# Optimization experiments

Hardware: AMD Instinct MI355X
Metric: run time of the kernel (lower is better)

The kernel has to match this reference:

```python
import jax, jax.numpy as jnp
import numpy as np

N, E, C_IN, H, K = 16384, 524288, 128, 64, 64


def setup_inputs() -> dict:
    key = jax.random.key(0)
    ks = jax.random.split(key, 6)
    x = jax.random.normal(ks[0], (N, C_IN), dtype=jnp.float32)
    edge_index = jax.random.randint(ks[1], (2, E), 0, N, dtype=jnp.int32)
    edge_weight = jax.random.uniform(ks[2], (E,), dtype=jnp.float32)
    sc = lambda f: 1.0 / np.sqrt(f)
    # GCNConv lin (no bias inside lin; separate bias), Glorot-ish init
    W1 = jax.random.normal(ks[3], (C_IN, H), dtype=jnp.float32) * sc(C_IN)
    b1 = jnp.zeros((H,), jnp.float32)
    # DMoNPooling MLP: Linear(H,H) then Linear(H,K), no activation between (act=None)
    Wm1 = jax.random.normal(ks[4], (H, H), dtype=jnp.float32) * sc(H)
    bm1 = jnp.zeros((H,), jnp.float32)
    Wm2 = jax.random.normal(ks[5], (H, K), dtype=jnp.float32) * sc(H)
    bm2 = jnp.zeros((K,), jnp.float32)
    return dict(x=x, edge_index=edge_index, edge_weight=edge_weight,
                W1=W1, b1=b1, Wm1=Wm1, bm1=bm1, Wm2=Wm2, bm2=bm2)


def gcn_conv(x, edge_index, edge_weight, W, b, n):
    # GCNConv: add self-loops (weight 1), symmetric deg^-1/2 normalization,
    # aggregate messages from source (row) into target (col).
    row, col = edge_index[0], edge_index[1]
    loop = jnp.arange(n, dtype=edge_index.dtype)
    row = jnp.concatenate([row, loop])
    col = jnp.concatenate([col, loop])
    w = jnp.concatenate([edge_weight, jnp.ones((n,), edge_weight.dtype)])
    deg = jax.ops.segment_sum(w, col, num_segments=n)
    dis = jnp.where(deg > 0, jax.lax.rsqrt(deg), 0.0)
    norm = dis[row] * w * dis[col]
    xw = x @ W  # [N, H]
    out = jax.ops.segment_sum(xw[row] * norm[:, None], col, num_segments=n)
    return out + b


def dmon_pool(h, adj, Wm1, bm1, Wm2, bm2):
    # eval mode: dropout disabled
    s = jax.nn.softmax((h @ Wm1 + bm1) @ Wm2 + bm2, axis=-1)  # [N, K]
    k = s.shape[-1]
    out_adj = s.T @ (adj @ s)  # [K, K]

    # Spectral (modularity) loss; degrees = einsum('ijk->ik', adj) = column sums
    deg = adj.sum(axis=0)  # [N]
    m = deg.sum() / 2
    ca = s.T @ deg  # [K], equals degrees^T s as well (symmetric roles)
    normalizer = jnp.outer(ca, ca) / 2 / m
    spectral_loss = -jnp.trace(out_adj - normalizer) / 2 / m

    # Orthogonality loss
    ss = s.T @ s  # [K, K]
    ss_fro = jnp.sqrt(jnp.sum(ss * ss))
    i_fro = jnp.sqrt(jnp.float32(k))  # ||I_K||_F
    diff = ss / ss_fro - jnp.eye(k, dtype=ss.dtype) / i_fro
    ortho_loss = jnp.sqrt(jnp.sum(diff * diff))

    # Cluster size loss
    cluster_size = s.sum(axis=0)  # [K]
    cluster_loss = jnp.sqrt(jnp.sum(cluster_size * cluster_size)) / h.shape[0] * i_fro - 1.0

    return s, spectral_loss, ortho_loss, cluster_loss


def reference(x, edge_index, edge_weight, W1, b1, Wm1, bm1, Wm2, bm2):
    h = jax.nn.relu(gcn_conv(x, edge_index, edge_weight, W1, b1, N))
    # to_dense_adj(edge_index): dense [N, N], duplicate edges summed
    adj = jnp.zeros((N, N), h.dtype).at[edge_index[0], edge_index[1]].add(1.0)
    s, spec, ortho, clus = dmon_pool(h, adj, Wm1, bm1, Wm2, bm2)
    return s[None], spec + ortho + clus
```

## Files before the change

### kernel.cpp

```cpp
#include <hip/hip_runtime.h>
#include <hip/hip_bf16.h>

typedef float          f4  __attribute__((ext_vector_type(4)));
typedef unsigned short us4 __attribute__((ext_vector_type(4)));
typedef int            i2  __attribute__((ext_vector_type(2)));

template <typename T>
__device__ __forceinline__ T ntload(const T* p) { return __builtin_nontemporal_load(p); }

__device__ __forceinline__ unsigned short f2bf(float f) {
    unsigned u = __float_as_uint(f);
    return (unsigned short)((u + 0x7FFF + ((u >> 16) & 1)) >> 16);
}
__device__ __forceinline__ float bf2f(unsigned short h) {
    return __uint_as_float((unsigned)h << 16);
}

__global__ __launch_bounds__(256) void k_degxw(const int* __restrict__ ei,
                      const float* __restrict__ ew,
                      unsigned long long* __restrict__ deg_rep,
                      const float* __restrict__ x, const float* __restrict__ W1,
                      float* __restrict__ xw, unsigned short* __restrict__ xw16,
                      int N, int E) {
    __shared__ float w1l[128 * 64];
    __shared__ f4    xt[16][32];
    if (blockIdx.x < 2048) {
        int e = blockIdx.x * 256 + threadIdx.x;
        if (e < E) {
            int c = ntload(ei + E + e);
            float w = ntload(ew + e);
            unsigned q = (unsigned)__float2uint_rn(w * 16777216.f);
            unsigned long long p = (1ULL << 40) | (unsigned long long)q;
            atomicAdd(&deg_rep[(size_t)(blockIdx.x & 7) * N + c], p);
        }
        return;
    }
    int xbid = blockIdx.x - 2048;
    for (int t = threadIdx.x; t < 128 * 64; t += 256) w1l[t] = W1[t];
    int lane = threadIdx.x & 63;
    int wv   = threadIdx.x >> 6;
    for (int base = xbid * 16; base < N; base += 512 * 16) {
        __syncthreads();
        for (int t = threadIdx.x; t < 16 * 32; t += 256)
            ((f4*)xt)[t] = ntload((const f4*)x + (size_t)base * 32 + t);
        __syncthreads();
        int r0 = wv * 4;
        float a0 = 0.f, a1 = 0.f, a2 = 0.f, a3 = 0.f;
#pragma unroll
        for (int q = 0; q < 32; ++q) {
            f4 x0 = xt[r0][q], x1 = xt[r0 + 1][q], x2 = xt[r0 + 2][q], x3 = xt[r0 + 3][q];
            float wa = w1l[(4 * q + 0) * 64 + lane];
            float wb = w1l[(4 * q + 1) * 64 + lane];
            float wc = w1l[(4 * q + 2) * 64 + lane];
            float wd = w1l[(4 * q + 3) * 64 + lane];
            a0 = fmaf(x0.x, wa, a0); a0 = fmaf(x0.y, wb, a0); a0 = fmaf(x0.z, wc, a0); a0 = fmaf(x0.w, wd, a0);
            a1 = fmaf(x1.x, wa, a1); a1 = fmaf(x1.y, wb, a1); a1 = fmaf(x1.z, wc, a1); a1 = fmaf(x1.w, wd, a1);
            a2 = fmaf(x2.x, wa, a2); a2 = fmaf(x2.y, wb, a2); a2 = fmaf(x2.z, wc, a2); a2 = fmaf(x2.w, wd, a2);
            a3 = fmaf(x3.x, wa, a3); a3 = fmaf(x3.y, wb, a3); a3 = fmaf(x3.z, wc, a3); a3 = fmaf(x3.w, wd, a3);
        }
        int gr = base + r0;
        __builtin_nontemporal_store(a0, xw + (size_t)(gr + 0) * 64 + lane);
        __builtin_nontemporal_store(a1, xw + (size_t)(gr + 1) * 64 + lane);
        __builtin_nontemporal_store(a2, xw + (size_t)(gr + 2) * 64 + lane);
        __builtin_nontemporal_store(a3, xw + (size_t)(gr + 3) * 64 + lane);
        xw16[(size_t)(gr + 0) * 64 + lane] = f2bf(a0);
        xw16[(size_t)(gr + 1) * 64 + lane] = f2bf(a1);
        xw16[(size_t)(gr + 2) * 64 + lane] = f2bf(a2);
        xw16[(size_t)(gr + 3) * 64 + lane] = f2bf(a3);
    }
}

__global__ void k_red(const unsigned long long* __restrict__ deg_rep,
                      int* __restrict__ off_rep, int* __restrict__ cnt,
                      float* __restrict__ dis, int N) {
    int c = blockIdx.x * blockDim.x + threadIdx.x;
    if (c >= N) return;
    int run = 0;
    unsigned long long wsum = 0;
#pragma unroll
    for (int rep = 0; rep < 8; ++rep) {
        unsigned long long p = deg_rep[(size_t)rep * N + c];
        off_rep[(size_t)rep * N + c] = run;
        run += (int)(p >> 40);
        wsum += (p & ((1ULL << 40) - 1));
    }
    cnt[c] = run;
    dis[c] = rsqrtf((float)wsum * (1.f / 16777216.f) + 1.0f);
}

__global__ void k_scan(const int* __restrict__ cnt, int* __restrict__ offs, int N) {
    __shared__ int part[1024];
    int tid = threadIdx.x;
    int C = (N + 1023) / 1024;
    int base = tid * C;
    int loc[16];
    int sum = 0;
#pragma unroll
    for (int i = 0; i < 16; ++i) {
        if (i < C) {
            int idx = base + i;
            loc[i] = sum;
            sum += (idx < N) ? cnt[idx] : 0;
        }
    }
    part[tid] = sum;
    __syncthreads();
    for (int o = 1; o < 1024; o <<= 1) {
        int t = (tid >= o) ? part[tid - o] : 0;
        __syncthreads();
        part[tid] += t;
        __syncthreads();
    }
    int excl = part[tid] - sum;
#pragma unroll
    for (int i = 0; i < 16; ++i) {
        if (i < C) {
            int idx = base + i;
            if (idx < N) offs[idx] = excl + loc[i];
        }
    }
    if (tid == 1023) offs[N] = part[tid];
}

__global__ void k_bucket(const int* __restrict__ ei, const float* __restrict__ ew,
                         const float* __restrict__ dis, const int* __restrict__ offs,
                         const int* __restrict__ off_rep, int* __restrict__ cursor_rep,
                         i2* __restrict__ barr, int N, int E) {
    int e = blockIdx.x * blockDim.x + threadIdx.x;
    if (e < E) {
        int rep = blockIdx.x & 7;
        int r = ntload(ei + e), c = ntload(ei + E + e);
        float norm = dis[r] * ntload(ew + e) * dis[c];
        size_t rc = (size_t)rep * N + c;
        int pos = offs[c] + off_rep[rc] + atomicAdd(&cursor_rep[rc], 1);
        i2 rec; rec.x = r; rec.y = __float_as_int(norm);
        barr[pos] = rec;
    }
}

__global__ __launch_bounds__(512) void k_gmlp(const int* __restrict__ offs,
                         const i2* __restrict__ barr,
                         const float* __restrict__ xw, const unsigned short* __restrict__ xw16,
                         const float* __restrict__ dis, const float* __restrict__ b1,
                         const float* __restrict__ Wm1, const float* __restrict__ bm1,
                         const float* __restrict__ Wm2, const float* __restrict__ bm2,
                         float* __restrict__ s, unsigned short* __restrict__ s16, int N) {
    __shared__ float w1m[4096], w2m[4096];
    __shared__ float tsc[8][2][64];
    for (int t = threadIdx.x; t < 4096; t += 512) { w1m[t] = Wm1[t]; w2m[t] = Wm2[t]; }
    __syncthreads();
    int lane = threadIdx.x & 63;
    int sub = lane >> 4, q = lane & 15;
    int wv   = threadIdx.x >> 6;
    int wid  = blockIdx.x * 8 + wv;
    int nw   = 8 * gridDim.x;
    const us4* xw16v = (const us4*)xw16;
    for (int cp = wid; cp < (N >> 1); cp += nw) {
        int c0 = 2 * cp, c1 = c0 + 1;
        int beg = ntload(offs + c0), mid = ntload(offs + c1), end = ntload(offs + c1 + 1);
        f4 A0 = {0.f, 0.f, 0.f, 0.f}, A1 = A0, B0 = A0, B1 = A0;
        for (int i = beg; i < end; i += 64) {
            int nloc = min(64, end - i);
            bool ok = (i + lane < end);
            i2 b = ok ? ntload(barr + i + lane) : (i2){0, 0};
            int   rv = b.x;
            float nv = __int_as_float(b.y);
            int jmax = (nloc + 3) >> 2;
            int j = 0;
            for (; j + 4 <= jmax; j += 4) {
                int e0 = 4 * j + sub;
                int g0 = i + e0;
                int   r0 = __shfl(rv, e0),      r1 = __shfl(rv, e0 + 4);
                int   r2 = __shfl(rv, e0 + 8),  r3 = __shfl(rv, e0 + 12);
                float n0 = __shfl(nv, e0),      n1 = __shfl(nv, e0 + 4);
                float n2 = __shfl(nv, e0 + 8),  n3 = __shfl(nv, e0 + 12);
                us4 u0 = xw16v[(size_t)r0 * 16 + q];
                us4 u1 = xw16v[(size_t)r1 * 16 + q];
                us4 u2 = xw16v[(size_t)r2 * 16 + q];
                us4 u3 = xw16v[(size_t)r3 * 16 + q];
                float a0w = (g0      < mid) ? n0 : 0.f, b0w = n0 - a0w;
                float a1w = (g0 + 4  < mid) ? n1 : 0.f, b1w = n1 - a1w;
                float a2w = (g0 + 8  < mid) ? n2 : 0.f, b2w = n2 - a2w;
                float a3w = (g0 + 12 < mid) ? n3 : 0.f, b3w = n3 - a3w;
                A0.x = fmaf(bf2f(u0.x), a0w, A0.x); A0.y = fmaf(bf2f(u0.y), a0w, A0.y);
                A0.z = fmaf(bf2f(u0.z), a0w, A0.z); A0.w = fmaf(bf2f(u0.w), a0w, A0.w);
                B0.x = fmaf(bf2f(u0.x), b0w, B0.x); B0.y = fmaf(bf2f(u0.y), b0w, B0.y);
                B0.z = fmaf(bf2f(u0.z), b0w, B0.z); B0.w = fmaf(bf2f(u0.w), b0w, B0.w);
                A1.x = fmaf(bf2f(u1.x), a1w, A1.x); A1.y = fmaf(bf2f(u1.y), a1w, A1.y);
                A1.z = fmaf(bf2f(u1.z), a1w, A1.z); A1.w = fmaf(bf2f(u1.w), a1w, A1.w);
                B1.x = fmaf(bf2f(u1.x), b1w, B1.x); B1.y = fmaf(bf2f(u1.y), b1w, B1.y);
                B1.z = fmaf(bf2f(u1.z), b1w, B1.z); B1.w = fmaf(bf2f(u1.w), b1w, B1.w);
                A0.x = fmaf(bf2f(u2.x), a2w, A0.x); A0.y = fmaf(bf2f(u2.y), a2w, A0.y);
                A0.z = fmaf(bf2f(u2.z), a2w, A0.z); A0.w = fmaf(bf2f(u2.w), a2w, A0.w);
                B0.x = fmaf(bf2f(u2.x), b2w, B0.x); B0.y = fmaf(bf2f(u2.y), b2w, B0.y);
                B0.z = fmaf(bf2f(u2.z), b2w, B0.z); B0.w = fmaf(bf2f(u2.w), b2w, B0.w);
                A1.x = fmaf(bf2f(u3.x), a3w, A1.x); A1.y = fmaf(bf2f(u3.y), a3w, A1.y);
                A1.z = fmaf(bf2f(u3.z), a3w, A1.z); A1.w = fmaf(bf2f(u3.w), a3w, A1.w);
                B1.x = fmaf(bf2f(u3.x), b3w, B1.x); B1.y = fmaf(bf2f(u3.y), b3w, B1.y);
                B1.z = fmaf(bf2f(u3.z), b3w, B1.z); B1.w = fmaf(bf2f(u3.w), b3w, B1.w);
            }
            for (; j < jmax; ++j) {
                int e = 4 * j + sub;
                int g = i + e;
                int   r  = __shfl(rv, e);
                float nm = __shfl(nv, e);
                us4 u = xw16v[(size_t)r * 16 + q];
                float aw = (g < mid) ? nm : 0.f, bw = nm - aw;
                A0.x = fmaf(bf2f(u.x), aw, A0.x); A0.y = fmaf(bf2f(u.y), aw, A0.y);
                A0.z = fmaf(bf2f(u.z), aw, A0.z); A0.w = fmaf(bf2f(u.w), aw, A0.w);
                B0.x = fmaf(bf2f(u.x), bw, B0.x); B0.y = fmaf(bf2f(u.y), bw, B0.y);
                B0.z = fmaf(bf2f(u.z), bw, B0.z); B0.w = fmaf(bf2f(u.w), bw, B0.w);
            }
        }
        A0.x += A1.x; A0.y += A1.y; A0.z += A1.z; A0.w += A1.w;
        B0.x += B1.x; B0.y += B1.y; B0.z += B1.z; B0.w += B1.w;
        A0.x += __shfl_xor(A0.x, 16); A0.y += __shfl_xor(A0.y, 16);
        A0.z += __shfl_xor(A0.z, 16); A0.w += __shfl_xor(A0.w, 16);
        B0.x += __shfl_xor(B0.x, 16); B0.y += __shfl_xor(B0.y, 16);
        B0.z += __shfl_xor(B0.z, 16); B0.w += __shfl_xor(B0.w, 16);
        A0.x += __shfl_xor(A0.x, 32); A0.y += __shfl_xor(A0.y, 32);
        A0.z += __shfl_xor(A0.z, 32); A0.w += __shfl_xor(A0.w, 32);
        B0.x += __shfl_xor(B0.x, 32); B0.y += __shfl_xor(B0.y, 32);
        B0.z += __shfl_xor(B0.z, 32); B0.w += __shfl_xor(B0.w, 32);
        f4 bb = ((const f4*)b1)[q];
        f4 self0 = ntload((const f4*)xw + (size_t)c0 * 16 + q);
        f4 self1 = ntload((const f4*)xw + (size_t)c1 * 16 + q);
        float d0 = dis[c0], d1 = dis[c1];
        float dd0 = d0 * d0, dd1 = d1 * d1;
        f4 v0, v1;
        v0.x = A0.x + self0.x * dd0 + bb.x; v0.y = A0.y + self0.y * dd0 + bb.y;
        v0.z = A0.z + self0.z * dd0 + bb.z; v0.w = A0.w + self0.w * dd0 + bb.w;
        v1.x = B0.x + self1.x * dd1 + bb.x; v1.y = B0.y + self1.y * dd1 + bb.y;
        v1.z = B0.z + self1.z * dd1 + bb.z; v1.w = B0.w + self1.w * dd1 + bb.w;
        v0.x = v0.x > 0.f ? v0.x : 0.f; v0.y = v0.y > 0.f ? v0.y : 0.f;
        v0.z = v0.z > 0.f ? v0.z : 0.f; v0.w = v0.w > 0.f ? v0.w : 0.f;
        v1.x = v1.x > 0.f ? v1.x : 0.f; v1.y = v1.y > 0.f ? v1.y : 0.f;
        v1.z = v1.z > 0.f ? v1.z : 0.f; v1.w = v1.w > 0.f ? v1.w : 0.f;
        float t0 = bm1[lane], t1 = t0;
#pragma unroll
        for (int k = 0; k < 16; ++k) {
            float wa = w1m[(4 * k + 0) * 64 + lane];
            float wb = w1m[(4 * k + 1) * 64 + lane];
            float wc = w1m[(4 * k + 2) * 64 + lane];
            float wd = w1m[(4 * k + 3) * 64 + lane];
            t0 = fmaf(__shfl(v0.x, k), wa, t0); t0 = fmaf(__shfl(v0.y, k), wb, t0);
            t0 = fmaf(__shfl(v0.z, k), wc, t0); t0 = fmaf(__shfl(v0.w, k), wd, t0);
            t1 = fmaf(__shfl(v1.x, k), wa, t1); t1 = fmaf(__shfl(v1.y, k), wb, t1);
            t1 = fmaf(__shfl(v1.z, k), wc, t1); t1 = fmaf(__shfl(v1.w, k), wd, t1);
        }
        tsc[wv][0][lane] = t0;
        tsc[wv][1][lane] = t1;
        float g0 = bm2[lane], g1 = g0;
#pragma unroll
        for (int k = 0; k < 16; ++k) {
            f4 ta = ((f4*)tsc[wv][0])[k];
            f4 tb = ((f4*)tsc[wv][1])[k];
            float wa = w2m[(4 * k + 0) * 64 + lane];
            float wb = w2m[(4 * k + 1) * 64 + lane];
            float wc = w2m[(4 * k + 2) * 64 + lane];
            float wd = w2m[(4 * k + 3) * 64 + lane];
            g0 = fmaf(ta.x, wa, g0); g0 = fmaf(ta.y, wb, g0);
            g0 = fmaf(ta.z, wc, g0); g0 = fmaf(ta.w, wd, g0);
            g1 = fmaf(tb.x, wa, g1); g1 = fmaf(tb.y, wb, g1);
            g1 = fmaf(tb.z, wc, g1); g1 = fmaf(tb.w, wd, g1);
        }
        float m0 = g0, m1 = g1;
#pragma unroll
        for (int o = 32; o > 0; o >>= 1) {
            m0 = fmaxf(m0, __shfl_xor(m0, o));
            m1 = fmaxf(m1, __shfl_xor(m1, o));
        }
        float e0 = __expf(g0 - m0), e1 = __expf(g1 - m1);
        float z0 = e0, z1 = e1;
#pragma unroll
        for (int o = 32; o > 0; o >>= 1) {
            z0 += __shfl_xor(z0, o);
            z1 += __shfl_xor(z1, o);
        }
        float o0 = e0 / z0, o1 = e1 / z1;
        __builtin_nontemporal_store(o0, s + (size_t)c0 * 64 + lane);
        __builtin_nontemporal_store(o1, s + (size_t)c1 * 64 + lane);
        s16[(size_t)c0 * 64 + lane] = f2bf(o0);
        s16[(size_t)c1 * 64 + lane] = f2bf(o1);
    }
}

__global__ __launch_bounds__(256) void k_rt(const int* __restrict__ offs,
                         const i2* __restrict__ barr,
                         const unsigned short* __restrict__ s16,
                         const float* __restrict__ s, const int* __restrict__ cnt,
                         float* __restrict__ ssg, float* __restrict__ cag,
                         float* __restrict__ csg, float* __restrict__ tracearr, int N) {
    __shared__ float tile[64][64];
    __shared__ float bsum;
    int lane = threadIdx.x & 63;
    int wv   = threadIdx.x >> 6;
    if (blockIdx.x >= 2048) {
        int base = (blockIdx.x - 2048) * 64;
        if (base >= N) return;
        for (int t = threadIdx.x; t < 1024; t += 256)
            ((f4*)tile)[t] = ntload((const f4*)(s + (size_t)base * 64) + t);
        __syncthreads();
        float acc[16];
#pragma unroll
        for (int i = 0; i < 16; ++i) acc[i] = 0.f;
        for (int r = 0; r < 64; ++r) {
            float sj = tile[r][lane];
            const float* brow = &tile[r][wv * 16];
#pragma unroll
            for (int i = 0; i < 16; ++i) acc[i] = fmaf(brow[i], sj, acc[i]);
        }
        float csj = 0.f, caj = 0.f;
#pragma unroll
        for (int i = 0; i < 16; ++i) {
            int r = wv * 16 + i;
            float sj = tile[r][lane];
            csj += sj;
            caj = fmaf(sj, (float)cnt[base + r], caj);
        }
#pragma unroll
        for (int i = 0; i < 16; ++i) atomicAdd(&ssg[(wv * 16 + i) * 64 + lane], acc[i]);
        atomicAdd(&csg[lane], csj);
        atomicAdd(&cag[lane], caj);
        return;
    }
    int sub = lane >> 4, q = lane & 15;
    int wid  = blockIdx.x * 4 + wv;
    int nw   = 4 * 2048;
    const us4* s16v = (const us4*)s16;
    float tacc = 0.f;
    for (int cp = wid; cp < (N >> 1); cp += nw) {
        int c0 = 2 * cp, c1 = c0 + 1;
        int beg = ntload(offs + c0), mid = ntload(offs + c1), end = ntload(offs + c1 + 1);
        us4 scu0 = s16v[(size_t)c0 * 16 + q];
        us4 scu1 = s16v[(size_t)c1 * 16 + q];
        f4 sc0 = {bf2f(scu0.x), bf2f(scu0.y), bf2f(scu0.z), bf2f(scu0.w)};
        f4 sc1 = {bf2f(scu1.x), bf2f(scu1.y), bf2f(scu1.z), bf2f(scu1.w)};
        f4 A0 = {0.f, 0.f, 0.f, 0.f}, A1 = A0, B0 = A0, B1 = A0;
        for (int i = beg; i < end; i += 64) {
            int nloc = min(64, end - i);
            int rv = (i + lane < end) ? ntload(barr + i + lane).x : 0;
            int jmax = (nloc + 3) >> 2;
            int j = 0;
            for (; j + 4 <= jmax; j += 4) {
                int e0 = 4 * j + sub;
                int g0 = i + e0;
                int r0 = __shfl(rv, e0),     r1 = __shfl(rv, e0 + 4);
                int r2 = __shfl(rv, e0 + 8), r3 = __shfl(rv, e0 + 12);
                float n0 = (e0      < nloc) ? 1.f : 0.f;
                float n1 = (e0 + 4  < nloc) ? 1.f : 0.f;
                float n2 = (e0 + 8  < nloc) ? 1.f : 0.f;
                float n3 = (e0 + 12 < nloc) ? 1.f : 0.f;
                us4 u0 = s16v[(size_t)r0 * 16 + q];
                us4 u1 = s16v[(size_t)r1 * 16 + q];
                us4 u2 = s16v[(size_t)r2 * 16 + q];
                us4 u3 = s16v[(size_t)r3 * 16 + q];
                float a0w = (g0      < mid) ? n0 : 0.f, b0w = n0 - a0w;
                float a1w = (g0 + 4  < mid) ? n1 : 0.f, b1w = n1 - a1w;
                float a2w = (g0 + 8  < mid) ? n2 : 0.f, b2w = n2 - a2w;
                float a3w = (g0 + 12 < mid) ? n3 : 0.f, b3w = n3 - a3w;
                A0.x = fmaf(bf2f(u0.x), a0w, A0.x); A0.y = fmaf(bf2f(u0.y), a0w, A0.y);
                A0.z = fmaf(bf2f(u0.z), a0w, A0.z); A0.w = fmaf(bf2f(u0.w), a0w, A0.w);
                B0.x = fmaf(bf2f(u0.x), b0w, B0.x); B0.y = fmaf(bf2f(u0.y), b0w, B0.y);
                B0.z = fmaf(bf2f(u0.z), b0w, B0.z); B0.w = fmaf(bf2f(u0.w), b0w, B0.w);
                A1.x = fmaf(bf2f(u1.x), a1w, A1.x); A1.y = fmaf(bf2f(u1.y), a1w, A1.y);
                A1.z = fmaf(bf2f(u1.z), a1w, A1.z); A1.w = fmaf(bf2f(u1.w), a1w, A1.w);
                B1.x = fmaf(bf2f(u1.x), b1w, B1.x); B1.y = fmaf(bf2f(u1.y), b1w, B1.y);
                B1.z = fmaf(bf2f(u1.z), b1w, B1.z); B1.w = fmaf(bf2f(u1.w), b1w, B1.w);
                A0.x = fmaf(bf2f(u2.x), a2w, A0.x); A0.y = fmaf(bf2f(u2.y), a2w, A0.y);
                A0.z = fmaf(bf2f(u2.z), a2w, A0.z); A0.w = fmaf(bf2f(u2.w), a2w, A0.w);
                B0.x = fmaf(bf2f(u2.x), b2w, B0.x); B0.y = fmaf(bf2f(u2.y), b2w, B0.y);
                B0.z = fmaf(bf2f(u2.z), b2w, B0.z); B0.w = fmaf(bf2f(u2.w), b2w, B0.w);
                A1.x = fmaf(bf2f(u3.x), a3w, A1.x); A1.y = fmaf(bf2f(u3.y), a3w, A1.y);
                A1.z = fmaf(bf2f(u3.z), a3w, A1.z); A1.w = fmaf(bf2f(u3.w), a3w, A1.w);
                B1.x = fmaf(bf2f(u3.x), b3w, B1.x); B1.y = fmaf(bf2f(u3.y), b3w, B1.y);
                B1.z = fmaf(bf2f(u3.z), b3w, B1.z); B1.w = fmaf(bf2f(u3.w), b3w, B1.w);
            }
            for (; j < jmax; ++j) {
                int e = 4 * j + sub;
                int g = i + e;
                int r = __shfl(rv, e);
                float m = (e < nloc) ? 1.f : 0.f;
                us4 u = s16v[(size_t)r * 16 + q];
                float aw = (g < mid) ? m : 0.f, bw = m - aw;
                A0.x = fmaf(bf2f(u.x), aw, A0.x); A0.y = fmaf(bf2f(u.y), aw, A0.y);
                A0.z = fmaf(bf2f(u.z), aw, A0.z); A0.w = fmaf(bf2f(u.w), aw, A0.w);
                B0.x = fmaf(bf2f(u.x), bw, B0.x); B0.y = fmaf(bf2f(u.y), bw, B0.y);
                B0.z = fmaf(bf2f(u.z), bw, B0.z); B0.w = fmaf(bf2f(u.w), bw, B0.w);
            }
        }
        A0.x += A1.x; A0.y += A1.y; A0.z += A1.z; A0.w += A1.w;
        B0.x += B1.x; B0.y += B1.y; B0.z += B1.z; B0.w += B1.w;
        A0.x += __shfl_xor(A0.x, 16); A0.y += __shfl_xor(A0.y, 16);
        A0.z += __shfl_xor(A0.z, 16); A0.w += __shfl_xor(A0.w, 16);
        B0.x += __shfl_xor(B0.x, 16); B0.y += __shfl_xor(B0.y, 16);
        B0.z += __shfl_xor(B0.z, 16); B0.w += __shfl_xor(B0.w, 16);
        A0.x += __shfl_xor(A0.x, 32); A0.y += __shfl_xor(A0.y, 32);
        A0.z += __shfl_xor(A0.z, 32); A0.w += __shfl_xor(A0.w, 32);
        B0.x += __shfl_xor(B0.x, 32); B0.y += __shfl_xor(B0.y, 32);
        B0.z += __shfl_xor(B0.z, 32); B0.w += __shfl_xor(B0.w, 32);
        tacc += A0.x * sc0.x + A0.y * sc0.y + A0.z * sc0.z + A0.w * sc0.w;
        tacc += B0.x * sc1.x + B0.y * sc1.y + B0.z * sc1.z + B0.w * sc1.w;
    }
    tacc *= 0.25f;
#pragma unroll
    for (int o = 32; o > 0; o >>= 1) tacc += __shfl_xor(tacc, o);
    if (threadIdx.x == 0) bsum = 0.f;
    __syncthreads();
    if (lane == 0) atomicAdd(&bsum, tacc);
    __syncthreads();
    if (threadIdx.x == 0) tracearr[blockIdx.x] = bsum;
}

__global__ void k_final(const float* __restrict__ ssg, const float* __restrict__ cag,
                        const float* __restrict__ csg, const float* __restrict__ tracearr,
                        int ntr, float Ef, float Nf, float* __restrict__ out) {
    __shared__ float red[256];
    int tid = threadIdx.x;

    float a = 0.f;
    for (int t = tid; t < ntr; t += 256) a += tracearr[t];
    red[tid] = a; __syncthreads();
    for (int o = 128; o > 0; o >>= 1) { if (tid < o) red[tid] += red[tid + o]; __syncthreads(); }
    float trace = red[0]; __syncthreads();

    a = 0.f;
    for (int t = tid; t < 4096; t += 256) { float v = ssg[t]; a += v * v; }
    red[tid] = a; __syncthreads();
    for (int o = 128; o > 0; o >>= 1) { if (tid < o) red[tid] += red[tid + o]; __syncthreads(); }
    float ss_sumsq = red[0]; __syncthreads();

    a = (tid < 64) ? ssg[tid * 64 + tid] : 0.f;
    red[tid] = a; __syncthreads();
    for (int o = 128; o > 0; o >>= 1) { if (tid < o) red[tid] += red[tid + o]; __syncthreads(); }
    float tr_ss = red[0]; __syncthreads();

    a = (tid < 64) ? cag[tid] * cag[tid] : 0.f;
    red[tid] = a; __syncthreads();
    for (int o = 128; o > 0; o >>= 1) { if (tid < o) red[tid] += red[tid + o]; __syncthreads(); }
    float ca_ss = red[0]; __syncthreads();

    a = (tid < 64) ? csg[tid] * csg[tid] : 0.f;
    red[tid] = a; __syncthreads();
    for (int o = 128; o > 0; o >>= 1) { if (tid < o) red[tid] += red[tid + o]; __syncthreads(); }
    float cs_ss = red[0];

    if (tid == 0) {
        float spec = -(trace - ca_ss / Ef) / Ef;
        float ss_fro = sqrtf(ss_sumsq);
        float ortho = sqrtf(fmaxf(2.f - tr_ss / (4.f * ss_fro), 0.f));
        float clus = sqrtf(cs_ss) / Nf * 8.f - 1.f;
        out[0] = spec + ortho + clus;
    }
}

extern "C" void kernel_launch(void* const* d_in, const int* in_sizes, int n_in,
                              void* d_out, int out_size, void* d_ws, size_t ws_size,
                              hipStream_t stream) {
    const float* x   = (const float*)d_in[0];
    const int*   ei  = (const int*)d_in[1];
    const float* ew  = (const float*)d_in[2];
    const float* W1  = (const float*)d_in[3];
    const float* b1  = (const float*)d_in[4];
    const float* Wm1 = (const float*)d_in[5];
    const float* bm1 = (const float*)d_in[6];
    const float* Wm2 = (const float*)d_in[7];
    const float* bm2 = (const float*)d_in[8];

    const int N = in_sizes[0] / 128;
    const int E = in_sizes[2];
    const int TGRID = 2304;

    char* base = (char*)d_ws;
    unsigned long long* deg_rep = (unsigned long long*)base;
    int*   cursor_rep = (int*)(base + (size_t)64 * N);
    float* ssg = (float*)(base + (size_t)96 * N);
    float* cag = ssg + 4096;
    float* csg = cag + 64;
    size_t zbytes = (size_t)96 * N + (4096 + 128) * 4;
    char* up = base + ((zbytes + 15) & ~(size_t)15);
    int*   cnt = (int*)up;            up += (size_t)4 * N;
    float* dis = (float*)up;          up += (size_t)4 * N;
    int*   offs = (int*)up;           up += (size_t)4 * (N + 1);
    float* tracearr = (float*)up;     up += (size_t)4 * 2048;
    up = (char*)(((size_t)up + 15) & ~(size_t)15);
    float* xw = (float*)up;           up += (size_t)4 * N * 64;
    int*   off_rep = (int*)up;        up += (size_t)32 * N;
    i2*    barr = (i2*)up;            up += (size_t)8 * E;
    unsigned short* xw16 = (unsigned short*)up; up += (size_t)2 * N * 64;
    unsigned short* s16  = (unsigned short*)up;
    float* sbuf = (float*)d_out;

    hipMemsetAsync(d_ws, 0, zbytes, stream);

    k_degxw<<<2560, 256, 0, stream>>>(ei, ew, deg_rep, x, W1, xw, xw16, N, E);
    k_red<<<(N + 255) / 256, 256, 0, stream>>>(deg_rep, off_rep, cnt, dis, N);
    k_scan<<<1, 1024, 0, stream>>>(cnt, offs, N);
    k_bucket<<<(E + 255) / 256, 256, 0, stream>>>(ei, ew, dis, offs, off_rep, cursor_rep, barr, N, E);
    k_gmlp<<<1024, 512, 0, stream>>>(offs, barr, xw, xw16, dis, b1, Wm1, bm1, Wm2, bm2, sbuf, s16, N);
    k_rt<<<TGRID, 256, 0, stream>>>(offs, barr, s16, sbuf, cnt, ssg, cag, csg, tracearr, N);
    k_final<<<1, 256, 0, stream>>>(ssg, cag, csg, tracearr, 2048, (float)E, (float)N,
                                   ((float*)d_out) + (size_t)N * 64);
}
```

Measured before the change: 242.5 us.

## Pack degree atomics to 32-bit, warp-shuffle scan, prefetch edge records, LDS broadcast in MLP

```diff
diff --git a/kernel.cpp b/kernel.cpp
--- a/kernel.cpp
+++ b/kernel.cpp
@@ -18,7 +18,7 @@
 
 __global__ __launch_bounds__(256) void k_degxw(const int* __restrict__ ei,
                       const float* __restrict__ ew,
-                      unsigned long long* __restrict__ deg_rep,
+                      unsigned* __restrict__ deg_rep,
                       const float* __restrict__ x, const float* __restrict__ W1,
                       float* __restrict__ xw, unsigned short* __restrict__ xw16,
                       int N, int E) {
@@ -29,9 +29,8 @@
         if (e < E) {
             int c = ntload(ei + E + e);
             float w = ntload(ew + e);
-            unsigned q = (unsigned)__float2uint_rn(w * 16777216.f);
-            unsigned long long p = (1ULL << 40) | (unsigned long long)q;
-            atomicAdd(&deg_rep[(size_t)(blockIdx.x & 7) * N + c], p);
+            unsigned q = __float2uint_rn(w * 524288.f);
+            atomicAdd(&deg_rep[(size_t)(blockIdx.x & 7) * N + c], (1u << 25) | q);
         }
         return;
     }
@@ -70,56 +69,56 @@
     }
 }
 
-__global__ void k_red(const unsigned long long* __restrict__ deg_rep,
+__global__ void k_red(const unsigned* __restrict__ deg_rep,
                       int* __restrict__ off_rep, int* __restrict__ cnt,
                       float* __restrict__ dis, int N) {
     int c = blockIdx.x * blockDim.x + threadIdx.x;
     if (c >= N) return;
     int run = 0;
-    unsigned long long wsum = 0;
+    unsigned wsum = 0;
 #pragma unroll
     for (int rep = 0; rep < 8; ++rep) {
-        unsigned long long p = deg_rep[(size_t)rep * N + c];
+        unsigned p = deg_rep[(size_t)rep * N + c];
         off_rep[(size_t)rep * N + c] = run;
-        run += (int)(p >> 40);
-        wsum += (p & ((1ULL << 40) - 1));
+        run += (int)(p >> 25);
+        wsum += (p & ((1u << 25) - 1));
     }
     cnt[c] = run;
-    dis[c] = rsqrtf((float)wsum * (1.f / 16777216.f) + 1.0f);
+    dis[c] = rsqrtf((float)wsum * (1.f / 524288.f) + 1.0f);
 }
 
 __global__ void k_scan(const int* __restrict__ cnt, int* __restrict__ offs, int N) {
-    __shared__ int part[1024];
+    __shared__ int wsum[16];
     int tid = threadIdx.x;
-    int C = (N + 1023) / 1024;
-    int base = tid * C;
+    int lane = tid & 63, wv = tid >> 6;
+    int base = tid * 16;
     int loc[16];
     int sum = 0;
 #pragma unroll
-    for (int i = 0; i < 16; ++i) {
-        if (i < C) {
-            int idx = base + i;
-            loc[i] = sum;
-            sum += (idx < N) ? cnt[idx] : 0;
-        }
-    }
-    part[tid] = sum;
+    for (int i = 0; i < 16; ++i) { loc[i] = sum; sum += cnt[base + i]; }
+    int s = sum;
+#pragma unroll
+    for (int o = 1; o < 64; o <<= 1) {
+        int t = __shfl_up(s, o);
+        if (lane >= o) s += t;
+    }
+    if (lane == 63) wsum[wv] = s;
     __syncthreads();
-    for (int o = 1; o < 1024; o <<= 1) {
-        int t = (tid >= o) ? part[tid - o] : 0;
-        __syncthreads();
-        part[tid] += t;
-        __syncthreads();
-    }
-    int excl = part[tid] - sum;
-#pragma unroll
-    for (int i = 0; i < 16; ++i) {
-        if (i < C) {
-            int idx = base + i;
-            if (idx < N) offs[idx] = excl + loc[i];
-        }
-    }
-    if (tid == 1023) offs[N] = part[tid];
+    if (wv == 0 && lane < 16) {
+        int ws = wsum[lane];
+        int ss = ws;
+#pragma unroll
+        for (int o = 1; o < 16; o <<= 1) {
+            int t = __shfl_up(ss, o);
+            if (lane >= o) ss += t;
+        }
+        wsum[lane] = ss - ws;
+    }
+    __syncthreads();
+    int excl = s - sum + wsum[wv];
+#pragma unroll
+    for (int i = 0; i < 16; ++i) offs[base + i] = excl + loc[i];
+    if (tid == 1023) offs[N] = excl + sum;
 }
 
 __global__ void k_bucket(const int* __restrict__ ei, const float* __restrict__ ew,
@@ -138,7 +137,7 @@
     }
 }
 
-__global__ __launch_bounds__(512) void k_gmlp(const int* __restrict__ offs,
+__global__ __launch_bounds__(512, 4) void k_gmlp(const int* __restrict__ offs,
                          const i2* __restrict__ barr,
                          const float* __restrict__ xw, const unsigned short* __restrict__ xw16,
                          const float* __restrict__ dis, const float* __restrict__ b1,
@@ -146,6 +145,7 @@
                          const float* __restrict__ Wm2, const float* __restrict__ bm2,
                          float* __restrict__ s, unsigned short* __restrict__ s16, int N) {
     __shared__ float w1m[4096], w2m[4096];
+    __shared__ float hsc[8][2][64];
     __shared__ float tsc[8][2][64];
     for (int t = threadIdx.x; t < 4096; t += 512) { w1m[t] = Wm1[t]; w2m[t] = Wm2[t]; }
     __syncthreads();
@@ -159,12 +159,15 @@
         int c0 = 2 * cp, c1 = c0 + 1;
         int beg = ntload(offs + c0), mid = ntload(offs + c1), end = ntload(offs + c1 + 1);
         f4 A0 = {0.f, 0.f, 0.f, 0.f}, A1 = A0, B0 = A0, B1 = A0;
-        for (int i = beg; i < end; i += 64) {
+        int i = beg;
+        i2 bcur = (beg + lane < end) ? ntload(barr + beg + lane) : (i2){0, 0};
+        while (i < end) {
+            int inext = i + 64;
+            i2 bnxt = {0, 0};
+            if (inext + lane < end) bnxt = ntload(barr + inext + lane);
             int nloc = min(64, end - i);
-            bool ok = (i + lane < end);
-            i2 b = ok ? ntload(barr + i + lane) : (i2){0, 0};
-            int   rv = b.x;
-            float nv = __int_as_float(b.y);
+            int   rv = bcur.x;
+            float nv = __int_as_float(bcur.y);
             int jmax = (nloc + 3) >> 2;
             int j = 0;
             for (; j + 4 <= jmax; j += 4) {
@@ -211,6 +214,8 @@
                 B0.x = fmaf(bf2f(u.x), bw, B0.x); B0.y = fmaf(bf2f(u.y), bw, B0.y);
                 B0.z = fmaf(bf2f(u.z), bw, B0.z); B0.w = fmaf(bf2f(u.w), bw, B0.w);
             }
+            i = inext;
+            bcur = bnxt;
         }
         A0.x += A1.x; A0.y += A1.y; A0.z += A1.z; A0.w += A1.w;
         B0.x += B1.x; B0.y += B1.y; B0.z += B1.z; B0.w += B1.w;
@@ -236,17 +241,23 @@
         v0.z = v0.z > 0.f ? v0.z : 0.f; v0.w = v0.w > 0.f ? v0.w : 0.f;
         v1.x = v1.x > 0.f ? v1.x : 0.f; v1.y = v1.y > 0.f ? v1.y : 0.f;
         v1.z = v1.z > 0.f ? v1.z : 0.f; v1.w = v1.w > 0.f ? v1.w : 0.f;
+        if (sub == 0) {
+            ((f4*)hsc[wv][0])[q] = v0;
+            ((f4*)hsc[wv][1])[q] = v1;
+        }
         float t0 = bm1[lane], t1 = t0;
 #pragma unroll
         for (int k = 0; k < 16; ++k) {
+            f4 ha = ((f4*)hsc[wv][0])[k];
+            f4 hb = ((f4*)hsc[wv][1])[k];
             float wa = w1m[(4 * k + 0) * 64 + lane];
             float wb = w1m[(4 * k + 1) * 64 + lane];
             float wc = w1m[(4 * k + 2) * 64 + lane];
             float wd = w1m[(4 * k + 3) * 64 + lane];
-            t0 = fmaf(__shfl(v0.x, k), wa, t0); t0 = fmaf(__shfl(v0.y, k), wb, t0);
-            t0 = fmaf(__shfl(v0.z, k), wc, t0); t0 = fmaf(__shfl(v0.w, k), wd, t0);
-            t1 = fmaf(__shfl(v1.x, k), wa, t1); t1 = fmaf(__shfl(v1.y, k), wb, t1);
-            t1 = fmaf(__shfl(v1.z, k), wc, t1); t1 = fmaf(__shfl(v1.w, k), wd, t1);
+            t0 = fmaf(ha.x, wa, t0); t0 = fmaf(ha.y, wb, t0);
+            t0 = fmaf(ha.z, wc, t0); t0 = fmaf(ha.w, wd, t0);
+            t1 = fmaf(hb.x, wa, t1); t1 = fmaf(hb.y, wb, t1);
+            t1 = fmaf(hb.z, wc, t1); t1 = fmaf(hb.w, wd, t1);
         }
         tsc[wv][0][lane] = t0;
         tsc[wv][1][lane] = t1;
@@ -337,9 +348,14 @@
         f4 sc0 = {bf2f(scu0.x), bf2f(scu0.y), bf2f(scu0.z), bf2f(scu0.w)};
         f4 sc1 = {bf2f(scu1.x), bf2f(scu1.y), bf2f(scu1.z), bf2f(scu1.w)};
         f4 A0 = {0.f, 0.f, 0.f, 0.f}, A1 = A0, B0 = A0, B1 = A0;
-        for (int i = beg; i < end; i += 64) {
+        int i = beg;
+        int rcur = (beg + lane < end) ? ntload(barr + beg + lane).x : 0;
+        while (i < end) {
+            int inext = i + 64;
+            int rnxt = 0;
+            if (inext + lane < end) rnxt = ntload(barr + inext + lane).x;
             int nloc = min(64, end - i);
-            int rv = (i + lane < end) ? ntload(barr + i + lane).x : 0;
+            int rv = rcur;
             int jmax = (nloc + 3) >> 2;
             int j = 0;
             for (; j + 4 <= jmax; j += 4) {
@@ -388,6 +404,8 @@
                 B0.x = fmaf(bf2f(u.x), bw, B0.x); B0.y = fmaf(bf2f(u.y), bw, B0.y);
                 B0.z = fmaf(bf2f(u.z), bw, B0.z); B0.w = fmaf(bf2f(u.w), bw, B0.w);
             }
+            i = inext;
+            rcur = rnxt;
         }
         A0.x += A1.x; A0.y += A1.y; A0.z += A1.z; A0.w += A1.w;
         B0.x += B1.x; B0.y += B1.y; B0.z += B1.z; B0.w += B1.w;
@@ -472,12 +490,12 @@
     const int TGRID = 2304;
 
     char* base = (char*)d_ws;
-    unsigned long long* deg_rep = (unsigned long long*)base;
-    int*   cursor_rep = (int*)(base + (size_t)64 * N);
-    float* ssg = (float*)(base + (size_t)96 * N);
+    unsigned* deg_rep = (unsigned*)base;
+    int*   cursor_rep = (int*)(base + (size_t)32 * N);
+    float* ssg = (float*)(base + (size_t)64 * N);
     float* cag = ssg + 4096;
     float* csg = cag + 64;
-    size_t zbytes = (size_t)96 * N + (4096 + 128) * 4;
+    size_t zbytes = (size_t)64 * N + (4096 + 128) * 4;
     char* up = base + ((zbytes + 15) & ~(size_t)15);
     int*   cnt = (int*)up;            up += (size_t)4 * N;
     float* dis = (float*)up;          up += (size_t)4 * N;
```

Result: slower. 269.4 us (+11.1%).
